# Kernel tuning notes

Measured on AMD Instinct MI355X. Metric: run time of the kernel, lower is better.

## Reference

```python
import jax, jax.numpy as jnp
import numpy as np

B, Q, LE, D, P, A = 8, 32, 128, 512, 32, 128


def setup_inputs() -> dict:
    key = jax.random.key(0)
    ks = jax.random.split(key, 8)
    exp_tokens = jax.random.normal(ks[0], (B, Q, LE, D), dtype=jnp.float32)
    exp_mask = jax.random.randint(ks[1], (B, Q, LE), 0, 2, dtype=jnp.int32)
    s_j = jax.random.normal(ks[2], (B, P, D), dtype=jnp.float32)
    req_mask = jax.random.randint(ks[3], (B, P), 0, 2, dtype=jnp.int32)
    sc = 1.0 / np.sqrt(D)
    Ws_w = jax.random.normal(ks[4], (A, D), dtype=jnp.float32) * sc
    Ws_b = jax.random.normal(ks[5], (A,), dtype=jnp.float32) * 0.01
    U_w = jax.random.normal(ks[6], (A, D), dtype=jnp.float32) * sc
    v_w = jax.random.normal(ks[7], (1, A), dtype=jnp.float32) * (1.0 / np.sqrt(A))
    return {"exp_tokens": exp_tokens, "exp_mask": exp_mask, "s_j": s_j,
            "req_mask": req_mask, "Ws_w": Ws_w, "Ws_b": Ws_b, "U_w": U_w, "v_w": v_w}


def reference(exp_tokens, exp_mask, s_j, req_mask, Ws_w, Ws_b, U_w, v_w):
    # ws: (B,P,A); uh: (B,Q,Le,A)
    ws = jnp.einsum('bpd,ad->bpa', s_j, Ws_w) + Ws_b
    uh = jnp.einsum('bqtd,ad->bqta', exp_tokens, U_w)
    # broadcast add -> (B,Q,P,Le,A), tanh, project with v -> (B,Q,P,Le)
    scored = jnp.tanh(uh[:, :, None, :, :] + ws[:, None, :, None, :])
    e = jnp.einsum('bqpta,a->bqpt', scored, v_w[0])
    tok_mask = exp_mask[:, :, None, :]  # (B,Q,1,Le) broadcast over P
    e = jnp.where(tok_mask == 0, jnp.float32(-1e9), e)
    # joint softmax over Q*Le per (b,p)
    e_t = jnp.transpose(e, (0, 2, 1, 3)).reshape(e.shape[0], e.shape[2], -1)
    a = jax.nn.softmax(e_t, axis=-1).reshape(e.shape[0], e.shape[2], e.shape[1], e.shape[3])
    a = jnp.transpose(a, (0, 2, 1, 3))  # (B,Q,P,Le)
    s_rlk = jnp.einsum('bqpt,bqtd->bqpd', a, exp_tokens)
    rmask = req_mask[:, None, :, None].astype(s_rlk.dtype)
    return s_rlk * rmask
```

## Files before the change

### kernel.cpp

```cpp
#include <hip/hip_runtime.h>
#include <hip/hip_bf16.h>

#define B_  8
#define Q_  32
#define LE_ 128
#define D_  512
#define P_  32
#define A_  128

typedef __attribute__((ext_vector_type(8))) short short8_t;
typedef __attribute__((ext_vector_type(4))) float floatx4_t;

typedef const __attribute__((address_space(1))) unsigned int glb_uint;
typedef __attribute__((address_space(3))) unsigned int lds_uint;
#define GLD16(g, s) __builtin_amdgcn_global_load_lds((glb_uint*)(g), (lds_uint*)(s), 16, 0, 0)

__device__ __forceinline__ short f2bf(float x) {
    unsigned u = __float_as_uint(x);
    unsigned r = (u + 0x7fffu + ((u >> 16) & 1u)) >> 16;
    return (short)r;
}
__device__ __forceinline__ float bf2f(short s) {
    return __uint_as_float(((unsigned)(unsigned short)s) << 16);
}
__device__ __forceinline__ short8_t cvt8(float4 a, float4 b) {
    short8_t s;
    s[0] = f2bf(a.x); s[1] = f2bf(a.y); s[2] = f2bf(a.z); s[3] = f2bf(a.w);
    s[4] = f2bf(b.x); s[5] = f2bf(b.y); s[6] = f2bf(b.z); s[7] = f2bf(b.w);
    return s;
}

__global__ __launch_bounds__(256) void prep_kernel(
    const float* __restrict__ W,
    const float* __restrict__ s_j, const float* __restrict__ Ws_w,
    const float* __restrict__ Ws_b,
    short* __restrict__ Wb,
    float* __restrict__ EW, float* __restrict__ gsums) {
    __shared__ float s_row[D_];
    int blk = blockIdx.x;
    int tid = threadIdx.x;
    if (blk < 256) {
        int bp = blk;
        if (blk == 0) gsums[tid] = 0.0f;
        const float* src = s_j + (size_t)bp * D_;
        for (int i = tid; i < D_; i += 256) s_row[i] = src[i];
        __syncthreads();
        if (tid < 128) {
            int a = tid;
            const float4* w4 = (const float4*)(Ws_w + (size_t)a * D_);
            const float4* s4 = (const float4*)s_row;
            float acc = 0.0f;
#pragma unroll 8
            for (int i = 0; i < D_ / 4; ++i) {
                float4 w = w4[i];
                acc += w.x * s4[i].x + w.y * s4[i].y + w.z * s4[i].z + w.w * s4[i].w;
            }
            EW[bp * A_ + a] = __expf(2.0f * (acc + Ws_b[a]));
        }
        return;
    }
    size_t g = (size_t)(blk - 256) * 256 + tid;
    const float4* s4 = (const float4*)(W + g * 8);
    float4 a = s4[0], b = s4[1];
    *(short8_t*)(Wb + g * 8) = cvt8(a, b);
}

#define EUP_ 136
#define EWP_ 132
#define WPP_ 136

__global__ __launch_bounds__(512, 1) void score_kernel(
    const float* __restrict__ X, const short* __restrict__ Wb,
    const float* __restrict__ EW, const float* __restrict__ v_w,
    const int* __restrict__ exp_mask, float* __restrict__ gsums,
    short* __restrict__ wglob) {
    __shared__ short uS[32768];
    __shared__ float ew_s[32 * EWP_];
    __shared__ short w_s[32 * WPP_];
    __shared__ float n2v[128];
    __shared__ int   mask_s[128];

    int bq = blockIdx.x;
    int b  = bq >> 5;
    int tid = threadIdx.x;
    int wave = tid >> 6, lane = tid & 63;
    int qd = lane >> 4, lr = lane & 15;

    int m0 = (wave >> 1) * 32, n0 = (wave & 1) * 64;
    int cB = lane & 7;
    int rowB0 = wave * 16 + (lane >> 3);

    int rowA = tid >> 2;
    int ksg  = (tid & 3) * 16;
    int cb0  = (tid & 3) * 2;
    int wcb0 = (cb0 ^ (rowA & 7)) * 8;
    int wcb1 = ((cb0 + 1) ^ (rowA & 7)) * 8;
    const float* xrow = X + (size_t)(bq * 128 + rowA) * D_ + ksg;
    int aoff = rowA * 64;

    floatx4_t acc[2][4];
#pragma unroll
    for (int i = 0; i < 2; ++i)
#pragma unroll
        for (int j = 0; j < 4; ++j) acc[i][j] = (floatx4_t){0.f, 0.f, 0.f, 0.f};

    {
        const float4* xs = (const float4*)xrow;
        float4 a0 = xs[0], a1 = xs[1], a2 = xs[2], a3 = xs[3];
        *(short8_t*)(uS + aoff + wcb0) = cvt8(a0, a1);
        *(short8_t*)(uS + aoff + wcb1) = cvt8(a2, a3);
#pragma unroll
        for (int u = 0; u < 2; ++u) {
            int n = rowB0 + u * 8;
            GLD16(Wb + (size_t)n * D_ + ((cB ^ (n & 7)) * 8),
                  uS + 16384 + (wave * 2 + u) * 512);
        }
    }
    __syncthreads();

    for (int kt = 0; kt < 8; ++kt) {
        int cur = (kt & 1) << 13;
        int nxt = cur ^ 8192;
        float4 xv0, xv1, xv2, xv3;
        if (kt < 7) {
            const float4* xs = (const float4*)(xrow + (kt + 1) * 64);
            xv0 = xs[0]; xv1 = xs[1]; xv2 = xs[2]; xv3 = xs[3];
#pragma unroll
            for (int u = 0; u < 2; ++u) {
                int n = rowB0 + u * 8;
                GLD16(Wb + (size_t)n * D_ + (kt + 1) * 64 + ((cB ^ (n & 7)) * 8),
                      uS + 16384 + nxt + (wave * 2 + u) * 512);
            }
        }
#pragma unroll
        for (int ks = 0; ks < 2; ++ks) {
            int cr = (ks * 4 + qd) ^ (lr & 7);
            short8_t af[2], bfr[4];
#pragma unroll
            for (int i = 0; i < 2; ++i)
                af[i] = *(const short8_t*)(uS + cur + (m0 + i * 16 + lr) * 64 + cr * 8);
#pragma unroll
            for (int j = 0; j < 4; ++j)
                bfr[j] = *(const short8_t*)(uS + 16384 + cur + (n0 + j * 16 + lr) * 64 + cr * 8);
#pragma unroll
            for (int i = 0; i < 2; ++i)
#pragma unroll
                for (int j = 0; j < 4; ++j)
                    acc[i][j] = __builtin_amdgcn_mfma_f32_16x16x32_bf16(af[i], bfr[j], acc[i][j], 0, 0, 0);
        }
        __syncthreads();
        if (kt < 7) {
            *(short8_t*)(uS + nxt + aoff + wcb0) = cvt8(xv0, xv1);
            *(short8_t*)(uS + nxt + aoff + wcb1) = cvt8(xv2, xv3);
            __syncthreads();
        }
    }

#pragma unroll
    for (int i = 0; i < 2; ++i)
#pragma unroll
        for (int j = 0; j < 4; ++j)
#pragma unroll
            for (int r = 0; r < 4; ++r) {
                int t = m0 + i * 16 + qd * 4 + r;
                int a = n0 + j * 16 + lr;
                uS[t * EUP_ + a] = f2bf(__expf(2.0f * acc[i][j][r]));
            }
#pragma unroll
    for (int u = 0; u < 2; ++u) {
        int c = tid * 2 + u;
        int p = c >> 5, seg = c & 31;
        *(float4*)&ew_s[p * EWP_ + seg * 4] =
            *(const float4*)&EW[(size_t)(b * P_ + p) * A_ + seg * 4];
    }
    if (tid < 32) {
        float4 v = *(const float4*)(v_w + tid * 4);
        v.x *= -2.0f; v.y *= -2.0f; v.z *= -2.0f; v.w *= -2.0f;
        *(float4*)&n2v[tid * 4] = v;
    }
    if (tid < 128) mask_s[tid] = exp_mask[bq * LE_ + tid];
    __syncthreads();

    {
        int t = tid & 127, pg = tid >> 7;
        float acc8[8];
#pragma unroll
        for (int j = 0; j < 8; ++j) acc8[j] = 0.0f;
        for (int a8 = 0; a8 < 16; ++a8) {
            short8_t e8 = *(const short8_t*)&uS[t * EUP_ + a8 * 8];
            float eu[8];
#pragma unroll
            for (int k = 0; k < 8; ++k) eu[k] = bf2f(e8[k]);
            float4 nv0 = *(const float4*)&n2v[a8 * 8];
            float4 nv1 = *(const float4*)&n2v[a8 * 8 + 4];
            float nv[8] = {nv0.x, nv0.y, nv0.z, nv0.w, nv1.x, nv1.y, nv1.z, nv1.w};
#pragma unroll
            for (int j = 0; j < 8; ++j) {
                int p = pg * 8 + j;
                float4 w0 = *(const float4*)&ew_s[p * EWP_ + a8 * 8];
                float4 w1 = *(const float4*)&ew_s[p * EWP_ + a8 * 8 + 4];
                float ww[8] = {w0.x, w0.y, w0.z, w0.w, w1.x, w1.y, w1.z, w1.w};
#pragma unroll
                for (int k = 0; k < 8; ++k)
                    acc8[j] = fmaf(nv[k], __builtin_amdgcn_rcpf(fmaf(eu[k], ww[k], 1.0f)), acc8[j]);
            }
        }
        int mk = mask_s[t];
        short* wg = wglob + (size_t)bq * (P_ * LE_);
#pragma unroll
        for (int j = 0; j < 8; ++j) {
            float ee = mk ? __expf(acc8[j]) : 0.0f;
            short v = f2bf(ee);
            w_s[(pg * 8 + j) * WPP_ + t] = v;
            wg[(pg * 8 + j) * LE_ + t] = v;
        }
    }
    __syncthreads();

    if (tid < 256) {
        int p = tid >> 3, seg = tid & 7;
        const short* src = w_s + p * WPP_ + seg * 16;
        float s = 0.0f;
#pragma unroll
        for (int k = 0; k < 16; ++k) s += bf2f(src[k]);
        s += __shfl_xor(s, 1);
        s += __shfl_xor(s, 2);
        s += __shfl_xor(s, 4);
        if (seg == 0) atomicAdd(&gsums[b * P_ + p], s);
    }
}

__global__ __launch_bounds__(512, 4) void pv_kernel(
    const float* __restrict__ X, const short* __restrict__ wglob,
    const float* __restrict__ gsums, const int* __restrict__ req_mask,
    float* __restrict__ out) {
    __shared__ short pvB[128 * EUP_];
    __shared__ float rm_s[32];

    int blk = blockIdx.x;
    int bq = blk >> 2, chunk = blk & 3;
    int b = bq >> 5;
    int d0 = chunk * 128;
    int tid = threadIdx.x;
    int wave = tid >> 6, lane = tid & 63;
    int qd = lane >> 4, lr = lane & 15;

    if (tid < 32) {
        int bp = b * P_ + tid;
        float g = gsums[bp];
        rm_s[tid] = req_mask[bp] ? __builtin_amdgcn_rcpf(g) : 0.0f;
    }

    const short* wg = wglob + (size_t)bq * (P_ * LE_);
    short8_t afv[2][4];
#pragma unroll
    for (int i = 0; i < 2; ++i)
#pragma unroll
        for (int ks = 0; ks < 4; ++ks)
            afv[i][ks] = *(const short8_t*)&wg[(i * 16 + lr) * LE_ + ks * 32 + qd * 8];

    int tt = tid >> 2, dseg = (tid & 3) * 32;
    const float4* g4 = (const float4*)(X + (size_t)(bq * 128 + tt) * D_ + d0 + dseg);
    float4 f0 = g4[0], f1 = g4[1], f2 = g4[2], f3 = g4[3];
    float4 f4 = g4[4], f5 = g4[5], f6 = g4[6], f7 = g4[7];
    short8_t xs0 = cvt8(f0, f1), xs1 = cvt8(f2, f3), xs2 = cvt8(f4, f5), xs3 = cvt8(f6, f7);
#pragma unroll
    for (int e = 0; e < 8; ++e) {
        pvB[(dseg + 0 + e) * EUP_ + tt]  = xs0[e];
        pvB[(dseg + 8 + e) * EUP_ + tt]  = xs1[e];
        pvB[(dseg + 16 + e) * EUP_ + tt] = xs2[e];
        pvB[(dseg + 24 + e) * EUP_ + tt] = xs3[e];
    }
    __syncthreads();

    floatx4_t accp[2];
    accp[0] = (floatx4_t){0.f, 0.f, 0.f, 0.f};
    accp[1] = (floatx4_t){0.f, 0.f, 0.f, 0.f};
#pragma unroll
    for (int ks = 0; ks < 4; ++ks) {
        short8_t bfr = *(const short8_t*)&pvB[(wave * 16 + lr) * EUP_ + ks * 32 + qd * 8];
        accp[0] = __builtin_amdgcn_mfma_f32_16x16x32_bf16(afv[0][ks], bfr, accp[0], 0, 0, 0);
        accp[1] = __builtin_amdgcn_mfma_f32_16x16x32_bf16(afv[1][ks], bfr, accp[1], 0, 0, 0);
    }
#pragma unroll
    for (int i = 0; i < 2; ++i)
#pragma unroll
        for (int r = 0; r < 4; ++r) {
            int p = i * 16 + qd * 4 + r;
            __builtin_nontemporal_store(
                accp[i][r] * rm_s[p],
                &out[((size_t)bq * P_ + p) * D_ + d0 + wave * 16 + lr]);
        }
}

extern "C" void kernel_launch(void* const* d_in, const int* in_sizes, int n_in,
                              void* d_out, int out_size, void* d_ws, size_t ws_size,
                              hipStream_t stream) {
    const float* exp_tokens = (const float*)d_in[0];
    const int*   exp_mask   = (const int*)d_in[1];
    const float* s_j        = (const float*)d_in[2];
    const int*   req_mask   = (const int*)d_in[3];
    const float* Ws_w       = (const float*)d_in[4];
    const float* Ws_b       = (const float*)d_in[5];
    const float* U_w        = (const float*)d_in[6];
    const float* v_w        = (const float*)d_in[7];
    float* out = (float*)d_out;

    float* EW    = (float*)d_ws;
    float* gsums = EW + B_ * P_ * A_;
    short* Wb    = (short*)(gsums + 256);
    short* wglob = Wb + (size_t)A_ * D_;

    prep_kernel<<<dim3(256 + 32), dim3(256), 0, stream>>>(
        U_w, s_j, Ws_w, Ws_b, Wb, EW, gsums);
    score_kernel<<<dim3(B_ * Q_), dim3(512), 0, stream>>>(
        exp_tokens, Wb, EW, v_w, exp_mask, gsums, wglob);
    pv_kernel<<<dim3(B_ * Q_ * 4), dim3(512), 0, stream>>>(
        exp_tokens, wglob, gsums, req_mask, out);
}
```

Baseline: 161.3 us.

## Split score kernel into uh GEMM and score-weight kernels for more parallelism

The fused score kernel, which ran 256 blocks of 512 threads at one block per CU, is split in two. A uh GEMM kernel runs 512 half-tile blocks and writes exp(2·uh) in bf16 to a global workspace. A scorew kernel then runs 1024 smaller blocks that compute tanh-scores, masked exp weights and atomic row sums. This is meant to raise occupancy and fill more of the CUs. The cost is an extra kernel launch and a global round trip of the intermediate activations.

```diff
diff --git a/kernel.cpp b/kernel.cpp
--- a/kernel.cpp
+++ b/kernel.cpp
@@ -29,6 +29,9 @@
     s[4] = f2bf(b.x); s[5] = f2bf(b.y); s[6] = f2bf(b.z); s[7] = f2bf(b.w);
     return s;
 }
+
+#define EUP_ 136
+#define EWP_ 132
 
 __global__ __launch_bounds__(256) void prep_kernel(
     const float* __restrict__ W,
@@ -65,38 +68,27 @@
     *(short8_t*)(Wb + g * 8) = cvt8(a, b);
 }
 
-#define EUP_ 136
-#define EWP_ 132
-#define WPP_ 136
-
-__global__ __launch_bounds__(512, 1) void score_kernel(
+__global__ __launch_bounds__(256, 3) void uh_kernel(
     const float* __restrict__ X, const short* __restrict__ Wb,
-    const float* __restrict__ EW, const float* __restrict__ v_w,
-    const int* __restrict__ exp_mask, float* __restrict__ gsums,
-    short* __restrict__ wglob) {
-    __shared__ short uS[32768];
-    __shared__ float ew_s[32 * EWP_];
-    __shared__ short w_s[32 * WPP_];
-    __shared__ float n2v[128];
-    __shared__ int   mask_s[128];
-
-    int bq = blockIdx.x;
-    int b  = bq >> 5;
+    short* __restrict__ EUg) {
+    __shared__ short uS[24576];
+
+    int blk = blockIdx.x;
+    int bq = blk >> 1, th = blk & 1;
     int tid = threadIdx.x;
     int wave = tid >> 6, lane = tid & 63;
     int qd = lane >> 4, lr = lane & 15;
-
     int m0 = (wave >> 1) * 32, n0 = (wave & 1) * 64;
-    int cB = lane & 7;
-    int rowB0 = wave * 16 + (lane >> 3);
 
     int rowA = tid >> 2;
-    int ksg  = (tid & 3) * 16;
     int cb0  = (tid & 3) * 2;
     int wcb0 = (cb0 ^ (rowA & 7)) * 8;
     int wcb1 = ((cb0 + 1) ^ (rowA & 7)) * 8;
-    const float* xrow = X + (size_t)(bq * 128 + rowA) * D_ + ksg;
+    const float* xrow = X + (size_t)(bq * 128 + th * 64 + rowA) * D_ + (tid & 3) * 16;
     int aoff = rowA * 64;
+
+    int cB = lane & 7;
+    int rB = wave * 8 + (lane >> 3);
 
     floatx4_t acc[2][4];
 #pragma unroll
@@ -110,26 +102,26 @@
         *(short8_t*)(uS + aoff + wcb0) = cvt8(a0, a1);
         *(short8_t*)(uS + aoff + wcb1) = cvt8(a2, a3);
 #pragma unroll
-        for (int u = 0; u < 2; ++u) {
-            int n = rowB0 + u * 8;
+        for (int u = 0; u < 4; ++u) {
+            int n = u * 32 + rB;
             GLD16(Wb + (size_t)n * D_ + ((cB ^ (n & 7)) * 8),
-                  uS + 16384 + (wave * 2 + u) * 512);
+                  uS + 4096 + (u * 32 + wave * 8) * 64);
         }
     }
     __syncthreads();
 
     for (int kt = 0; kt < 8; ++kt) {
-        int cur = (kt & 1) << 13;
-        int nxt = cur ^ 8192;
+        int cur = (kt & 1) * 12288;
+        int nxt = cur ^ 12288;
         float4 xv0, xv1, xv2, xv3;
         if (kt < 7) {
             const float4* xs = (const float4*)(xrow + (kt + 1) * 64);
             xv0 = xs[0]; xv1 = xs[1]; xv2 = xs[2]; xv3 = xs[3];
 #pragma unroll
-            for (int u = 0; u < 2; ++u) {
-                int n = rowB0 + u * 8;
+            for (int u = 0; u < 4; ++u) {
+                int n = u * 32 + rB;
                 GLD16(Wb + (size_t)n * D_ + (kt + 1) * 64 + ((cB ^ (n & 7)) * 8),
-                      uS + 16384 + nxt + (wave * 2 + u) * 512);
+                      uS + nxt + 4096 + (u * 32 + wave * 8) * 64);
             }
         }
 #pragma unroll
@@ -141,7 +133,7 @@
                 af[i] = *(const short8_t*)(uS + cur + (m0 + i * 16 + lr) * 64 + cr * 8);
 #pragma unroll
             for (int j = 0; j < 4; ++j)
-                bfr[j] = *(const short8_t*)(uS + 16384 + cur + (n0 + j * 16 + lr) * 64 + cr * 8);
+                bfr[j] = *(const short8_t*)(uS + cur + 4096 + (n0 + j * 16 + lr) * 64 + cr * 8);
 #pragma unroll
             for (int i = 0; i < 2; ++i)
 #pragma unroll
@@ -156,6 +148,7 @@
         }
     }
 
+    size_t base = ((size_t)bq * 128 + th * 64) * 128;
 #pragma unroll
     for (int i = 0; i < 2; ++i)
 #pragma unroll
@@ -164,11 +157,35 @@
             for (int r = 0; r < 4; ++r) {
                 int t = m0 + i * 16 + qd * 4 + r;
                 int a = n0 + j * 16 + lr;
-                uS[t * EUP_ + a] = f2bf(__expf(2.0f * acc[i][j][r]));
+                EUg[base + (size_t)t * 128 + a] = f2bf(__expf(2.0f * acc[i][j][r]));
             }
-#pragma unroll
-    for (int u = 0; u < 2; ++u) {
-        int c = tid * 2 + u;
+}
+
+__global__ __launch_bounds__(256, 4) void scorew_kernel(
+    const short* __restrict__ EUg, const float* __restrict__ EW,
+    const float* __restrict__ v_w, const int* __restrict__ exp_mask,
+    float* __restrict__ gsums, short* __restrict__ wglob) {
+    __shared__ short eu_s[32 * EUP_];
+    __shared__ float ew_s[32 * EWP_];
+    __shared__ float n2v[128];
+    __shared__ int   mask_s[32];
+
+    int blk = blockIdx.x;
+    int bq = blk >> 2, t0 = (blk & 3) * 32;
+    int b  = bq >> 5;
+    int tid = threadIdx.x;
+    int lane = tid & 63;
+
+    {
+        int row = tid >> 3, seg = tid & 7;
+        const short8_t* src = (const short8_t*)(EUg + ((size_t)bq * 128 + t0 + row) * 128 + seg * 16);
+        short8_t v0 = src[0], v1 = src[1];
+        *(short8_t*)&eu_s[row * EUP_ + seg * 16] = v0;
+        *(short8_t*)&eu_s[row * EUP_ + seg * 16 + 8] = v1;
+    }
+#pragma unroll
+    for (int u = 0; u < 4; ++u) {
+        int c = tid * 4 + u;
         int p = c >> 5, seg = c & 31;
         *(float4*)&ew_s[p * EWP_ + seg * 4] =
             *(const float4*)&EW[(size_t)(b * P_ + p) * A_ + seg * 4];
@@ -177,56 +194,52 @@
         float4 v = *(const float4*)(v_w + tid * 4);
         v.x *= -2.0f; v.y *= -2.0f; v.z *= -2.0f; v.w *= -2.0f;
         *(float4*)&n2v[tid * 4] = v;
-    }
-    if (tid < 128) mask_s[tid] = exp_mask[bq * LE_ + tid];
+        mask_s[tid] = exp_mask[bq * LE_ + t0 + tid];
+    }
     __syncthreads();
 
-    {
-        int t = tid & 127, pg = tid >> 7;
-        float acc8[8];
-#pragma unroll
-        for (int j = 0; j < 8; ++j) acc8[j] = 0.0f;
-        for (int a8 = 0; a8 < 16; ++a8) {
-            short8_t e8 = *(const short8_t*)&uS[t * EUP_ + a8 * 8];
-            float eu[8];
-#pragma unroll
-            for (int k = 0; k < 8; ++k) eu[k] = bf2f(e8[k]);
-            float4 nv0 = *(const float4*)&n2v[a8 * 8];
-            float4 nv1 = *(const float4*)&n2v[a8 * 8 + 4];
-            float nv[8] = {nv0.x, nv0.y, nv0.z, nv0.w, nv1.x, nv1.y, nv1.z, nv1.w};
-#pragma unroll
-            for (int j = 0; j < 8; ++j) {
-                int p = pg * 8 + j;
-                float4 w0 = *(const float4*)&ew_s[p * EWP_ + a8 * 8];
-                float4 w1 = *(const float4*)&ew_s[p * EWP_ + a8 * 8 + 4];
-                float ww[8] = {w0.x, w0.y, w0.z, w0.w, w1.x, w1.y, w1.z, w1.w};
-#pragma unroll
-                for (int k = 0; k < 8; ++k)
-                    acc8[j] = fmaf(nv[k], __builtin_amdgcn_rcpf(fmaf(eu[k], ww[k], 1.0f)), acc8[j]);
-            }
-        }
-        int mk = mask_s[t];
-        short* wg = wglob + (size_t)bq * (P_ * LE_);
-#pragma unroll
-        for (int j = 0; j < 8; ++j) {
-            float ee = mk ? __expf(acc8[j]) : 0.0f;
-            short v = f2bf(ee);
-            w_s[(pg * 8 + j) * WPP_ + t] = v;
-            wg[(pg * 8 + j) * LE_ + t] = v;
-        }
-    }
-    __syncthreads();
-
-    if (tid < 256) {
-        int p = tid >> 3, seg = tid & 7;
-        const short* src = w_s + p * WPP_ + seg * 16;
-        float s = 0.0f;
-#pragma unroll
-        for (int k = 0; k < 16; ++k) s += bf2f(src[k]);
+    int t = tid & 31, pg = tid >> 5;
+    float acc4[4];
+#pragma unroll
+    for (int j = 0; j < 4; ++j) acc4[j] = 0.0f;
+    for (int a8 = 0; a8 < 16; ++a8) {
+        short8_t e8 = *(const short8_t*)&eu_s[t * EUP_ + a8 * 8];
+        float eu[8];
+#pragma unroll
+        for (int k = 0; k < 8; ++k) eu[k] = bf2f(e8[k]);
+        float4 nv0 = *(const float4*)&n2v[a8 * 8];
+        float4 nv1 = *(const float4*)&n2v[a8 * 8 + 4];
+        float nv[8] = {nv0.x, nv0.y, nv0.z, nv0.w, nv1.x, nv1.y, nv1.z, nv1.w};
+#pragma unroll
+        for (int j = 0; j < 4; ++j) {
+            int p = pg * 4 + j;
+            float4 w0 = *(const float4*)&ew_s[p * EWP_ + a8 * 8];
+            float4 w1 = *(const float4*)&ew_s[p * EWP_ + a8 * 8 + 4];
+            float ww[8] = {w0.x, w0.y, w0.z, w0.w, w1.x, w1.y, w1.z, w1.w};
+#pragma unroll
+            for (int k = 0; k < 8; ++k)
+                acc4[j] = fmaf(nv[k], __builtin_amdgcn_rcpf(fmaf(eu[k], ww[k], 1.0f)), acc4[j]);
+        }
+    }
+    int mk = mask_s[t];
+    short* wg = wglob + (size_t)bq * (P_ * LE_);
+    float sums[4];
+#pragma unroll
+    for (int j = 0; j < 4; ++j) {
+        float ee = mk ? __expf(acc4[j]) : 0.0f;
+        short v = f2bf(ee);
+        wg[(pg * 4 + j) * LE_ + t0 + t] = v;
+        sums[j] = bf2f(v);
+    }
+#pragma unroll
+    for (int j = 0; j < 4; ++j) {
+        float s = sums[j];
         s += __shfl_xor(s, 1);
         s += __shfl_xor(s, 2);
         s += __shfl_xor(s, 4);
-        if (seg == 0) atomicAdd(&gsums[b * P_ + p], s);
+        s += __shfl_xor(s, 8);
+        s += __shfl_xor(s, 16);
+        if ((lane & 31) == 0) atomicAdd(&gsums[b * P_ + pg * 4 + j], s);
     }
 }
 
@@ -310,11 +323,14 @@
     float* gsums = EW + B_ * P_ * A_;
     short* Wb    = (short*)(gsums + 256);
     short* wglob = Wb + (size_t)A_ * D_;
+    short* EUg   = wglob + (size_t)B_ * Q_ * P_ * LE_;
 
     prep_kernel<<<dim3(256 + 32), dim3(256), 0, stream>>>(
         U_w, s_j, Ws_w, Ws_b, Wb, EW, gsums);
-    score_kernel<<<dim3(B_ * Q_), dim3(512), 0, stream>>>(
-        exp_tokens, Wb, EW, v_w, exp_mask, gsums, wglob);
+    uh_kernel<<<dim3(B_ * Q_ * 2), dim3(256), 0, stream>>>(
+        exp_tokens, Wb, EUg);
+    scorew_kernel<<<dim3(B_ * Q_ * 4), dim3(256), 0, stream>>>(
+        EUg, EW, v_w, exp_mask, gsums, wglob);
     pv_kernel<<<dim3(B_ * Q_ * 4), dim3(512), 0, stream>>>(
         exp_tokens, wglob, gsums, req_mask, out);
 }
```

Result: slower. 189.8 us (+17.7%).
